# Kernel optimization log

Measured on AMD Instinct MI355X. Metric: run time of the kernel, lower is better.

Reference implementation:

```python
import jax, jax.numpy as jnp
import numpy as np

B, S, D, H = 2, 4096, 512, 8
HD = D // H
SCALE = float(np.sqrt(HD))


def setup_inputs() -> dict:
    key = jax.random.key(0)
    ks = jax.random.split(key, 11)
    std = 1.0 / np.sqrt(D)
    inp = {
        "query": jax.random.normal(ks[0], (B, S, D), jnp.float32),
        "key": jax.random.normal(ks[1], (B, S, D), jnp.float32),
        "value": jax.random.normal(ks[2], (B, S, D), jnp.float32),
        "Wq": jax.random.normal(ks[3], (D, D), jnp.float32) * std,
        "bq": jnp.zeros((D,), jnp.float32),
        "Wk": jax.random.normal(ks[4], (D, D), jnp.float32) * std,
        "bk": jnp.zeros((D,), jnp.float32),
        "Wv": jax.random.normal(ks[5], (D, D), jnp.float32) * std,
        "bv": jnp.zeros((D,), jnp.float32),
        "Wo": jax.random.normal(ks[6], (D, D), jnp.float32) * std,
        "bo": jnp.zeros((D,), jnp.float32),
    }
    return inp


def reference(query, key, value, Wq, bq, Wk, bk, Wv, bv, Wo, bo):
    # Linear projections, split into heads: [B, H, S, HD]
    def proj(x, W, b):
        y = jnp.einsum('bsd,df->bsf', x, W) + b
        return y.reshape(B, -1, H, HD).transpose(0, 2, 1, 3)

    Q = proj(query, Wq, bq)
    K = proj(key, Wk, bk)
    V = proj(value, Wv, bv)

    # Full [B, H, S, S] score matrix (faithful to the naive original)
    scores = jnp.einsum('bhqd,bhkd->bhqk', Q, K) / SCALE
    attn = jax.nn.softmax(scores, axis=-1)  # dropout = identity in eval
    attended = jnp.einsum('bhqk,bhkd->bhqd', attn, V)
    attended = attended.transpose(0, 2, 1, 3).reshape(B, -1, D)
    return jnp.einsum('bsd,df->bsf', attended, Wo) + bo
```

## Files before the change

### kernel.cpp

```cpp
#include <hip/hip_runtime.h>

typedef short short8 __attribute__((ext_vector_type(8)));
typedef short short4v __attribute__((ext_vector_type(4)));
typedef float f32x4 __attribute__((ext_vector_type(4)));
typedef float f32x16 __attribute__((ext_vector_type(16)));
typedef unsigned uint2v __attribute__((ext_vector_type(2)));

typedef __attribute__((address_space(1))) void gvoid;
typedef __attribute__((address_space(3))) void lvoid;

#define DEV static __device__ __forceinline__

constexpr int Dm = 512;
constexpr int Sm = 4096;
constexpr int Hh = 8;
constexpr long NTe = (long)2 * Sm * Dm;

#define QSCALE 0.18033688011112042f

DEV short f2bf(float f) {
  union { float f; unsigned u; } v; v.f = f;
  unsigned r = v.u + 0x7FFFu + ((v.u >> 16) & 1u);
  return (short)(r >> 16);
}

DEV float bf2f(short s) {
  unsigned u = ((unsigned)(unsigned short)s) << 16;
  union { unsigned u; float f; } v; v.u = u;
  return v.f;
}

DEV float exp2_fast(float x) {
#if __has_builtin(__builtin_amdgcn_exp2f)
  return __builtin_amdgcn_exp2f(x);
#else
  return exp2f(x);
#endif
}

DEV float max3f(float a, float b, float c) { return fmaxf(fmaxf(a, b), c); }

DEV unsigned cvt_pk_bf16(float lo, float hi) {
  unsigned r;
  asm("v_cvt_pk_bf16_f32 %0, %1, %2" : "=v"(r) : "v"(lo), "v"(hi));
  return r;
}

DEV int fr(int r) { return (r & 7) ^ (((r >> 3) & 1) << 2); }

DEV uint2v pl32swap(unsigned a, unsigned b) {
  return __builtin_amdgcn_permlane32_swap(a, b, false, false);
}
DEV float swap_max(float x) { return fmaxf(x, __shfl_xor(x, 32, 64)); }
DEV float swap_add(float x) { return x + __shfl_xor(x, 32, 64); }

DEV void async16(const void* g, void* l) {
  __builtin_amdgcn_global_load_lds((gvoid*)g, (lvoid*)l, 16, 0, 0);
}

__global__ __launch_bounds__(256) void cast_qkv(
    const float* __restrict__ q, const float* __restrict__ k,
    const float* __restrict__ v, short* __restrict__ xq,
    short* __restrict__ xk, short* __restrict__ xv) {
  int t = blockIdx.y;
  const float* src = (t == 0) ? q : (t == 1) ? k : v;
  short* dst = (t == 0) ? xq : (t == 1) ? xk : xv;
  long i = (long)(blockIdx.x * 256 + threadIdx.x) * 4;
  float4 f = *(const float4*)(src + i);
  short4v o;
  o[0] = f2bf(f.x); o[1] = f2bf(f.y); o[2] = f2bf(f.z); o[3] = f2bf(f.w);
  *(short4v*)(dst + i) = o;
}

__global__ __launch_bounds__(256) void wtrans(
    const float* __restrict__ wq, const float* __restrict__ wk,
    const float* __restrict__ wv, const float* __restrict__ wo,
    short* __restrict__ wt) {
  __shared__ short T[64 * 72];
  const int tid = threadIdx.x;
  const int n0 = blockIdx.x * 64, k0 = blockIdx.y * 64, w = blockIdx.z;
  const float* W = (w == 0) ? wq : (w == 1) ? wk : (w == 2) ? wv : wo;
  for (int t = 0; t < 4; ++t) {
    int flat = t * 256 + tid;
    int r = flat >> 4, c4 = flat & 15;
    float4 f = *(const float4*)(W + (k0 + r) * 512 + n0 + c4 * 4);
    T[(c4 * 4 + 0) * 72 + r] = f2bf(f.x);
    T[(c4 * 4 + 1) * 72 + r] = f2bf(f.y);
    T[(c4 * 4 + 2) * 72 + r] = f2bf(f.z);
    T[(c4 * 4 + 3) * 72 + r] = f2bf(f.w);
  }
  __syncthreads();
  for (int t = 0; t < 2; ++t) {
    int flat = t * 256 + tid;
    int r = flat >> 3, c = flat & 7;
    short8 v = *(const short8*)(T + r * 72 + c * 8);
    *(short8*)(wt + ((long)w << 18) + (n0 + r) * 512 + k0 + c * 8) = v;
  }
}

__global__ __launch_bounds__(256) void vtrans(
    const short* __restrict__ V, short* __restrict__ VT) {
  __shared__ short T[64 * 72];
  const int tid = threadIdx.x;
  const int s0 = blockIdx.x * 64, d0 = blockIdx.y * 64, b = blockIdx.z;
  for (int t = 0; t < 2; ++t) {
    int flat = t * 256 + tid;
    int sl = flat >> 3, c = flat & 7;
    short8 v = *(const short8*)(V + ((long)b * Sm + s0 + sl) * Dm + d0 + c * 8);
    for (int j = 0; j < 8; ++j) T[(c * 8 + j) * 72 + sl] = v[j];
  }
  __syncthreads();
  for (int t = 0; t < 2; ++t) {
    int flat = t * 256 + tid;
    int dl = flat >> 3, c = flat & 7;
    short8 v = *(const short8*)(T + dl * 72 + c * 8);
    *(short8*)(VT + ((long)b * Dm + d0 + dl) * Sm + s0 + c * 8) = v;
  }
}

template <bool OUT_BF16>
DEV void gemm_body(const short* __restrict__ A, const short* __restrict__ Bt,
                   const float* __restrict__ bias, float scale,
                   void* __restrict__ Yv, short* As, short* Bs) {
  constexpr int K = 512, N = 512, BK = 64;
  const int tid = threadIdx.x, lane = tid & 63, w = tid >> 6;
  const int lm = lane & 15, lg = lane >> 4;
  const int wr = w >> 1, wc = w & 1;
  const long bm = (long)blockIdx.y * 128;
  const long bn = (long)blockIdx.x * 128;
  f32x4 zero = {0.f, 0.f, 0.f, 0.f};
  f32x4 acc[4][4];
  for (int m = 0; m < 4; ++m)
    for (int n = 0; n < 4; ++n) acc[m][n] = zero;
  for (int k0 = 0; k0 < K; k0 += BK) {
    __syncthreads();
    for (int t = 0; t < 4; ++t) {
      int flat = t * 256 + tid;
      int row = flat >> 3, c = flat & 7;
      async16(A + (bm + row) * K + k0 + ((c ^ fr(row)) * 8), As + flat * 8);
    }
    for (int t = 0; t < 4; ++t) {
      int flat = t * 256 + tid;
      int row = flat >> 3, c = flat & 7;
      async16(Bt + (bn + row) * K + k0 + ((c ^ fr(row)) * 8), Bs + flat * 8);
    }
    __syncthreads();
    for (int kk = 0; kk < 2; ++kk) {
      short8 a[4], b[4];
      for (int m = 0; m < 4; ++m)
        a[m] = *(const short8*)(As + (wr * 64 + m * 16 + lm) * BK +
                                ((kk * 4 + lg) ^ fr(lm)) * 8);
      for (int n = 0; n < 4; ++n)
        b[n] = *(const short8*)(Bs + (wc * 64 + n * 16 + lm) * BK +
                                ((kk * 4 + lg) ^ fr(lm)) * 8);
      for (int m = 0; m < 4; ++m)
        for (int n = 0; n < 4; ++n)
          acc[m][n] = __builtin_amdgcn_mfma_f32_16x16x32_bf16(a[m], b[n], acc[m][n], 0, 0, 0);
    }
  }
  for (int m = 0; m < 4; ++m)
    for (int n = 0; n < 4; ++n) {
      long row0 = bm + wr * 64 + m * 16 + lg * 4;
      int col = (int)bn + wc * 64 + n * 16 + lm;
      float bb = bias[col];
      for (int j = 0; j < 4; ++j) {
        float val = (acc[m][n][j] + bb) * scale;
        if (OUT_BF16)
          ((short*)Yv)[(row0 + j) * N + col] = f2bf(val);
        else
          ((float*)Yv)[(row0 + j) * N + col] = val;
      }
    }
}

__global__ __launch_bounds__(256) void gemm_proj(
    const short* __restrict__ Xq, const short* __restrict__ Xk,
    const short* __restrict__ Xv, const short* __restrict__ Wt,
    const float* __restrict__ bq, const float* __restrict__ bk,
    const float* __restrict__ bv, short* __restrict__ Qb,
    short* __restrict__ Kb, short* __restrict__ Vb) {
  __shared__ short As[128 * 64];
  __shared__ short Bs[128 * 64];
  int z = blockIdx.z;
  const short* A = (z == 0) ? Xq : (z == 1) ? Xk : Xv;
  const short* Bt = Wt + (long)z * 512 * 512;
  const float* bias = (z == 0) ? bq : (z == 1) ? bk : bv;
  short* Y = (z == 0) ? Qb : (z == 1) ? Kb : Vb;
  float scale = (z == 0) ? QSCALE : 1.f;
  gemm_body<true>(A, Bt, bias, scale, Y, As, Bs);
}

__global__ __launch_bounds__(256) void gemm_out(
    const short* __restrict__ A, const short* __restrict__ Bt,
    const float* __restrict__ bias, float* __restrict__ Y) {
  __shared__ short As[128 * 64];
  __shared__ short Bs[128 * 64];
  gemm_body<false>(A, Bt, bias, 1.f, Y, As, Bs);
}

template <int NSPLIT>
__global__ __launch_bounds__(256) void attn(
    const short* __restrict__ Qb, const short* __restrict__ Kb,
    const short* __restrict__ VTb, short* __restrict__ Op0,
    short* __restrict__ OpRest, float2* __restrict__ Ml) {
  __shared__ short Ks[2][64 * 64];
  __shared__ short Vt[2][64 * 64];
  const int tid = threadIdx.x, lane = tid & 63, w = tid >> 6;
  const int q32 = lane & 31, l5 = lane >> 5;
  const int bh = blockIdx.y, b = bh >> 3, h = bh & 7;
  const int z = blockIdx.z;
  constexpr int KVLEN = Sm / NSPLIT;
  const int kvbase = z * KVLEN;
  const long baseQ = (long)b * Sm * Dm + h * 64;
  const long baseVT = ((long)b * Dm + h * 64) * Sm;
  const int q0w = blockIdx.x * 128 + w * 32;

  short8 qf[4];
#pragma unroll
  for (int ks = 0; ks < 4; ++ks)
    qf[ks] = *(const short8*)(Qb + baseQ + (long)(q0w + q32) * Dm + ks * 16 + l5 * 8);

  f32x16 o0, o1;
#pragma unroll
  for (int r = 0; r < 16; ++r) { o0[r] = 0.f; o1[r] = 0.f; }
  float mrun = -1e30f, lrun = 0.f;

  const int r0 = tid >> 3, c0 = tid & 7;
  const int r1 = 32 + (tid >> 3);
  const short* gk0 = Kb + baseQ + (long)(kvbase + r0) * Dm + (c0 ^ fr(r0)) * 8;
  const short* gk1 = Kb + baseQ + (long)(kvbase + r1) * Dm + (c0 ^ fr(r1)) * 8;
  const short* gv0 = VTb + baseVT + (long)r0 * Sm + kvbase + (c0 ^ fr(r0)) * 8;
  const short* gv1 = VTb + baseVT + (long)r1 * Sm + kvbase + (c0 ^ fr(r1)) * 8;
  const int l0 = tid * 8, l1 = (256 + tid) * 8;

  async16(gk0, &Ks[0][l0]); async16(gk1, &Ks[0][l1]);
  async16(gv0, &Vt[0][l0]); async16(gv1, &Vt[0][l1]);
  gk0 += 64 * Dm; gk1 += 64 * Dm; gv0 += 64; gv1 += 64;
  __syncthreads();

  const int cxor = fr(q32);

  constexpr int NTILES = KVLEN / 64;
  for (int it = 0; it < NTILES; ++it) {
    const int cur = it & 1;
    if (it + 1 < NTILES) {
      async16(gk0, &Ks[cur ^ 1][l0]); async16(gk1, &Ks[cur ^ 1][l1]);
      async16(gv0, &Vt[cur ^ 1][l0]); async16(gv1, &Vt[cur ^ 1][l1]);
      gk0 += 64 * Dm; gk1 += 64 * Dm; gv0 += 64; gv1 += 64;
    }

    f32x16 sc0, sc1;
#pragma unroll
    for (int r = 0; r < 16; ++r) { sc0[r] = 0.f; sc1[r] = 0.f; }
    __builtin_amdgcn_s_setprio(1);
#pragma unroll
    for (int ks = 0; ks < 4; ++ks) {
      int cx = (2 * ks + l5) ^ cxor;
      short8 kf0 = *(const short8*)(&Ks[cur][q32 * 64 + cx * 8]);
      short8 kf1 = *(const short8*)(&Ks[cur][(32 + q32) * 64 + cx * 8]);
      sc0 = __builtin_amdgcn_mfma_f32_32x32x16_bf16(kf0, qf[ks], sc0, 0, 0, 0);
      sc1 = __builtin_amdgcn_mfma_f32_32x32x16_bf16(kf1, qf[ks], sc1, 0, 0, 0);
    }
    __builtin_amdgcn_s_setprio(0);

    float t1 = max3f(sc0[0], sc0[1], sc0[2]);
    float t2 = max3f(sc0[3], sc0[4], sc0[5]);
    float t3 = max3f(sc0[6], sc0[7], sc0[8]);
    float t4 = max3f(sc0[9], sc0[10], sc0[11]);
    float t5 = max3f(sc0[12], sc0[13], sc0[14]);
    float ma = max3f(max3f(t1, t2, t3), max3f(t4, t5, sc0[15]), sc1[0]);
    t1 = max3f(sc1[1], sc1[2], sc1[3]);
    t2 = max3f(sc1[4], sc1[5], sc1[6]);
    t3 = max3f(sc1[7], sc1[8], sc1[9]);
    t4 = max3f(sc1[10], sc1[11], sc1[12]);
    t5 = max3f(sc1[13], sc1[14], sc1[15]);
    float tmax = fmaxf(ma, max3f(max3f(t1, t2, t3), t4, t5));
    tmax = swap_max(tmax);

    if (__any(tmax > mrun + 8.f)) {
      float mi = fmaxf(mrun, tmax);
      float cc = exp2_fast(mrun - mi);
      mrun = mi;
      lrun *= cc;
#pragma unroll
      for (int r = 0; r < 16; ++r) {
        float ccr = __shfl(cc, ((r & 3) + 8 * (r >> 2)) + 4 * l5, 32);
        o0[r] *= ccr;
        o1[r] *= ccr;
      }
    }

    float la[4] = {0.f, 0.f, 0.f, 0.f}, lb[4] = {0.f, 0.f, 0.f, 0.f};
#pragma unroll
    for (int r = 0; r < 16; ++r) {
      sc0[r] = exp2_fast(sc0[r] - mrun); la[r & 3] += sc0[r];
      sc1[r] = exp2_fast(sc1[r] - mrun); lb[r & 3] += sc1[r];
    }
    lrun += ((la[0] + la[1]) + (la[2] + la[3])) +
            ((lb[0] + lb[1]) + (lb[2] + lb[3]));

    __builtin_amdgcn_s_setprio(1);
#pragma unroll
    for (int kc = 0; kc < 4; ++kc) {
      const f32x16& sch = (kc < 2) ? sc0 : sc1;
      const int bb = 8 * (kc & 1);
      unsigned A = cvt_pk_bf16(sch[bb + 0], sch[bb + 1]);
      unsigned B = cvt_pk_bf16(sch[bb + 2], sch[bb + 3]);
      unsigned C = cvt_pk_bf16(sch[bb + 4], sch[bb + 5]);
      unsigned D = cvt_pk_bf16(sch[bb + 6], sch[bb + 7]);
      uint2v rac = pl32swap(A, C);
      uint2v rbd = pl32swap(B, D);
      union { unsigned u[4]; short8 s; } pu;
      pu.u[0] = rac[0]; pu.u[1] = rbd[0]; pu.u[2] = rac[1]; pu.u[3] = rbd[1];
      int cx = (2 * kc + l5) ^ cxor;
      short8 vf0 = *(const short8*)(&Vt[cur][q32 * 64 + cx * 8]);
      short8 vf1 = *(const short8*)(&Vt[cur][(32 + q32) * 64 + cx * 8]);
      o0 = __builtin_amdgcn_mfma_f32_32x32x16_bf16(pu.s, vf0, o0, 0, 0, 0);
      o1 = __builtin_amdgcn_mfma_f32_32x32x16_bf16(pu.s, vf1, o1, 0, 0, 0);
    }
    __builtin_amdgcn_s_setprio(0);
    __syncthreads();
  }

  lrun = swap_add(lrun);

  short* Op = (z == 0) ? Op0 : OpRest + (long)(z - 1) * NTe;
#pragma unroll
  for (int r = 0; r < 16; ++r) {
    int q = (r & 3) + 8 * (r >> 2) + 4 * l5;
    long rowoff = baseQ + (long)(q0w + q) * Dm;
    Op[rowoff + q32] = f2bf(o0[r]);
    Op[rowoff + 32 + q32] = f2bf(o1[r]);
  }
  if (l5 == 0) {
    float2 ml; ml.x = mrun; ml.y = lrun;
    Ml[(long)(z * 16 + bh) * Sm + q0w + q32] = ml;
  }
}

template <int NSPLIT>
__global__ __launch_bounds__(256) void mergeN(
    const short* __restrict__ Op0, const short* __restrict__ OpRest,
    const float2* __restrict__ Ml, short* __restrict__ Ob) {
  long idx = (long)blockIdx.x * 256 + threadIdx.x;
  long row = idx >> 6;
  int c8 = (int)(idx & 63);
  int col = c8 * 8;
  int h = col >> 6;
  int b = (int)(row >> 12);
  int s = (int)(row & 4095);
  int bh = b * 8 + h;
  float2 ml[NSPLIT];
  float M = -3e38f;
#pragma unroll
  for (int z = 0; z < NSPLIT; ++z) {
    ml[z] = Ml[(long)(z * 16 + bh) * Sm + s];
    M = fmaxf(M, ml[z].x);
  }
  float wz[NSPLIT], den = 0.f;
#pragma unroll
  for (int z = 0; z < NSPLIT; ++z) {
    wz[z] = exp2_fast(ml[z].x - M);
    den += ml[z].y * wz[z];
  }
  float inv = 1.0f / den;
  long off = row * 512 + col;
  float acc[8];
#pragma unroll
  for (int i = 0; i < 8; ++i) acc[i] = 0.f;
#pragma unroll
  for (int z = 0; z < NSPLIT; ++z) {
    const short* Op = (z == 0) ? Op0 : OpRest + (long)(z - 1) * NTe;
    short8 v = *(const short8*)(Op + off);
#pragma unroll
    for (int i = 0; i < 8; ++i) acc[i] += bf2f(v[i]) * wz[z];
  }
  short8 o;
#pragma unroll
  for (int i = 0; i < 8; ++i) o[i] = f2bf(acc[i] * inv);
  *(short8*)(Ob + off) = o;
}

extern "C" void kernel_launch(void* const* d_in, const int* in_sizes, int n_in,
                              void* d_out, int out_size, void* d_ws, size_t ws_size,
                              hipStream_t stream) {
  const float* query = (const float*)d_in[0];
  const float* key_  = (const float*)d_in[1];
  const float* value = (const float*)d_in[2];
  const float* Wq = (const float*)d_in[3]; const float* bq = (const float*)d_in[4];
  const float* Wk = (const float*)d_in[5]; const float* bk = (const float*)d_in[6];
  const float* Wv = (const float*)d_in[7]; const float* bv = (const float*)d_in[8];
  const float* Wo = (const float*)d_in[9]; const float* bo = (const float*)d_in[10];

  short* Xq = (short*)d_ws;
  short* Xk = Xq + NTe;
  short* Xv = Xk + NTe;
  short* Wt = Xv + NTe;
  short* Qb = Wt + 4 * 512 * 512;
  short* Kb = Qb + NTe;
  short* Vb = Kb + NTe;
  short* VT = Xv;
  short* Op0 = Xq;
  short* OpRest = Vb + NTe;
  short* Ob = Vb;

  const size_t base_bytes = (size_t)(6 * NTe + 4 * 512 * 512) * 2;
  const size_t need4 = base_bytes + 3 * (size_t)NTe * 2 + (size_t)4 * 16 * Sm * 8;
  const int nsplit = (ws_size >= need4) ? 4 : 2;
  float2* Ml = (float2*)(OpRest + (size_t)(nsplit - 1) * NTe);

  cast_qkv<<<dim3(4096, 3), 256, 0, stream>>>(query, key_, value, Xq, Xk, Xv);
  wtrans<<<dim3(8, 8, 4), 256, 0, stream>>>(Wq, Wk, Wv, Wo, Wt);

  gemm_proj<<<dim3(4, 64, 3), 256, 0, stream>>>(Xq, Xk, Xv, Wt, bq, bk, bv,
                                                Qb, Kb, Vb);

  vtrans<<<dim3(Sm / 64, Dm / 64, 2), 256, 0, stream>>>(Vb, VT);

  if (nsplit == 4) {
    attn<4><<<dim3(Sm / 128, 2 * Hh, 4), 256, 0, stream>>>(Qb, Kb, VT, Op0,
                                                           OpRest, Ml);
    mergeN<4><<<dim3((2 * Sm * 512 / 8) / 256), 256, 0, stream>>>(Op0, OpRest,
                                                                  Ml, Ob);
  } else {
    attn<2><<<dim3(Sm / 128, 2 * Hh, 2), 256, 0, stream>>>(Qb, Kb, VT, Op0,
                                                           OpRest, Ml);
    mergeN<2><<<dim3((2 * Sm * 512 / 8) / 256), 256, 0, stream>>>(Op0, OpRest,
                                                                  Ml, Ob);
  }

  gemm_out<<<dim3(4, 64), 256, 0, stream>>>(Ob, Wt + 3L * 512 * 512, bo,
                                            (float*)d_out);
}
```

Baseline: 179.2 us.

## Fuse split-KV merge into output projection GEMM A-tile load

Removes the separate mergeN kernel and its bf16 round-trip by merging the split-KV partial outputs with log-sum-exp weights directly while loading the A tile of the output projection GEMM. Also defers the cross-half max shuffle in attention to inside the rescale branch. The fused GEMM now loads A synchronously with per-row merge math that is recomputed once per N-tile (4x redundant reads of partials and Ml), trading a launch and an intermediate write/read for extra loads and less overlap.

After: 190.7 us. 1.06x slower.

```diff
diff --git a/kernel.cpp b/kernel.cpp
--- a/kernel.cpp
+++ b/kernel.cpp
@@ -190,12 +190,89 @@
   gemm_body<true>(A, Bt, bias, scale, Y, As, Bs);
 }
 
-__global__ __launch_bounds__(256) void gemm_out(
-    const short* __restrict__ A, const short* __restrict__ Bt,
+template <int NSPLIT>
+__global__ __launch_bounds__(256) void gemm_out_fused(
+    const short* __restrict__ Op0, const short* __restrict__ OpRest,
+    const float2* __restrict__ Ml, const short* __restrict__ Bt,
     const float* __restrict__ bias, float* __restrict__ Y) {
+  constexpr int K = 512, N = 512, BK = 64;
   __shared__ short As[128 * 64];
   __shared__ short Bs[128 * 64];
-  gemm_body<false>(A, Bt, bias, 1.f, Y, As, Bs);
+  const int tid = threadIdx.x, lane = tid & 63, w = tid >> 6;
+  const int lm = lane & 15, lg = lane >> 4;
+  const int wr = w >> 1, wc = w & 1;
+  const long bm = (long)blockIdx.y * 128;
+  const long bn = (long)blockIdx.x * 128;
+  f32x4 zero = {0.f, 0.f, 0.f, 0.f};
+  f32x4 acc[4][4];
+  for (int m = 0; m < 4; ++m)
+    for (int n = 0; n < 4; ++n) acc[m][n] = zero;
+  for (int k0 = 0; k0 < K; k0 += BK) {
+    __syncthreads();
+    const int hh = k0 >> 6;
+    for (int t = 0; t < 4; ++t) {
+      int flat = t * 256 + tid;
+      int row = flat >> 3, c = flat & 7;
+      long grow = bm + row;
+      int s = (int)(grow & (Sm - 1));
+      int bh = (int)(grow >> 12) * 8 + hh;
+      float2 ml[NSPLIT];
+      float M = -3e38f;
+#pragma unroll
+      for (int z = 0; z < NSPLIT; ++z) {
+        ml[z] = Ml[(long)(z * 16 + bh) * Sm + s];
+        M = fmaxf(M, ml[z].x);
+      }
+      float wz[NSPLIT], den = 0.f;
+#pragma unroll
+      for (int z = 0; z < NSPLIT; ++z) {
+        wz[z] = exp2_fast(ml[z].x - M);
+        den += ml[z].y * wz[z];
+      }
+      float inv = 1.0f / den;
+      long aoff = grow * 512 + k0 + ((c ^ fr(row)) * 8);
+      float accm[8];
+#pragma unroll
+      for (int i = 0; i < 8; ++i) accm[i] = 0.f;
+#pragma unroll
+      for (int z = 0; z < NSPLIT; ++z) {
+        const short* Op = (z == 0) ? Op0 : OpRest + (long)(z - 1) * NTe;
+        short8 v = *(const short8*)(Op + aoff);
+#pragma unroll
+        for (int i = 0; i < 8; ++i) accm[i] += bf2f(v[i]) * wz[z];
+      }
+      short8 o;
+#pragma unroll
+      for (int i = 0; i < 8; ++i) o[i] = f2bf(accm[i] * inv);
+      *(short8*)(As + flat * 8) = o;
+    }
+    for (int t = 0; t < 4; ++t) {
+      int flat = t * 256 + tid;
+      int row = flat >> 3, c = flat & 7;
+      async16(Bt + (bn + row) * K + k0 + ((c ^ fr(row)) * 8), Bs + flat * 8);
+    }
+    __syncthreads();
+    for (int kk = 0; kk < 2; ++kk) {
+      short8 a[4], b[4];
+      for (int m = 0; m < 4; ++m)
+        a[m] = *(const short8*)(As + (wr * 64 + m * 16 + lm) * BK +
+                                ((kk * 4 + lg) ^ fr(lm)) * 8);
+      for (int n = 0; n < 4; ++n)
+        b[n] = *(const short8*)(Bs + (wc * 64 + n * 16 + lm) * BK +
+                                ((kk * 4 + lg) ^ fr(lm)) * 8);
+      for (int m = 0; m < 4; ++m)
+        for (int n = 0; n < 4; ++n)
+          acc[m][n] = __builtin_amdgcn_mfma_f32_16x16x32_bf16(a[m], b[n], acc[m][n], 0, 0, 0);
+    }
+  }
+  for (int m = 0; m < 4; ++m)
+    for (int n = 0; n < 4; ++n) {
+      long row0 = bm + wr * 64 + m * 16 + lg * 4;
+      int col = (int)bn + wc * 64 + n * 16 + lm;
+      float bb = bias[col];
+      for (int j = 0; j < 4; ++j)
+        Y[(row0 + j) * N + col] = acc[m][n][j] + bb;
+    }
 }
 
 template <int NSPLIT>
@@ -274,10 +351,10 @@
     t3 = max3f(sc1[7], sc1[8], sc1[9]);
     t4 = max3f(sc1[10], sc1[11], sc1[12]);
     t5 = max3f(sc1[13], sc1[14], sc1[15]);
-    float tmax = fmaxf(ma, max3f(max3f(t1, t2, t3), t4, t5));
-    tmax = swap_max(tmax);
-
-    if (__any(tmax > mrun + 8.f)) {
+    float tmax_lane = fmaxf(ma, max3f(max3f(t1, t2, t3), t4, t5));
+
+    if (__any(tmax_lane > mrun + 8.f)) {
+      float tmax = swap_max(tmax_lane);
       float mi = fmaxf(mrun, tmax);
       float cc = exp2_fast(mrun - mi);
       mrun = mi;
@@ -338,49 +415,6 @@
   }
 }
 
-template <int NSPLIT>
-__global__ __launch_bounds__(256) void mergeN(
-    const short* __restrict__ Op0, const short* __restrict__ OpRest,
-    const float2* __restrict__ Ml, short* __restrict__ Ob) {
-  long idx = (long)blockIdx.x * 256 + threadIdx.x;
-  long row = idx >> 6;
-  int c8 = (int)(idx & 63);
-  int col = c8 * 8;
-  int h = col >> 6;
-  int b = (int)(row >> 12);
-  int s = (int)(row & 4095);
-  int bh = b * 8 + h;
-  float2 ml[NSPLIT];
-  float M = -3e38f;
-#pragma unroll
-  for (int z = 0; z < NSPLIT; ++z) {
-    ml[z] = Ml[(long)(z * 16 + bh) * Sm + s];
-    M = fmaxf(M, ml[z].x);
-  }
-  float wz[NSPLIT], den = 0.f;
-#pragma unroll
-  for (int z = 0; z < NSPLIT; ++z) {
-    wz[z] = exp2_fast(ml[z].x - M);
-    den += ml[z].y * wz[z];
-  }
-  float inv = 1.0f / den;
-  long off = row * 512 + col;
-  float acc[8];
-#pragma unroll
-  for (int i = 0; i < 8; ++i) acc[i] = 0.f;
-#pragma unroll
-  for (int z = 0; z < NSPLIT; ++z) {
-    const short* Op = (z == 0) ? Op0 : OpRest + (long)(z - 1) * NTe;
-    short8 v = *(const short8*)(Op + off);
-#pragma unroll
-    for (int i = 0; i < 8; ++i) acc[i] += bf2f(v[i]) * wz[z];
-  }
-  short8 o;
-#pragma unroll
-  for (int i = 0; i < 8; ++i) o[i] = f2bf(acc[i] * inv);
-  *(short8*)(Ob + off) = o;
-}
-
 extern "C" void kernel_launch(void* const* d_in, const int* in_sizes, int n_in,
                               void* d_out, int out_size, void* d_ws, size_t ws_size,
                               hipStream_t stream) {
@@ -402,7 +436,6 @@
   short* VT = Xv;
   short* Op0 = Xq;
   short* OpRest = Vb + NTe;
-  short* Ob = Vb;
 
   const size_t base_bytes = (size_t)(6 * NTe + 4 * 512 * 512) * 2;
   const size_t need4 = base_bytes + 3 * (size_t)NTe * 2 + (size_t)4 * 16 * Sm * 8;
@@ -420,15 +453,12 @@
   if (nsplit == 4) {
     attn<4><<<dim3(Sm / 128, 2 * Hh, 4), 256, 0, stream>>>(Qb, Kb, VT, Op0,
                                                            OpRest, Ml);
-    mergeN<4><<<dim3((2 * Sm * 512 / 8) / 256), 256, 0, stream>>>(Op0, OpRest,
-                                                                  Ml, Ob);
+    gemm_out_fused<4><<<dim3(4, 64), 256, 0, stream>>>(
+        Op0, OpRest, Ml, Wt + 3L * 512 * 512, bo, (float*)d_out);
   } else {
     attn<2><<<dim3(Sm / 128, 2 * Hh, 2), 256, 0, stream>>>(Qb, Kb, VT, Op0,
                                                            OpRest, Ml);
-    mergeN<2><<<dim3((2 * Sm * 512 / 8) / 256), 256, 0, stream>>>(Op0, OpRest,
-                                                                  Ml, Ob);
-  }
-
-  gemm_out<<<dim3(4, 64), 256, 0, stream>>>(Ob, Wt + 3L * 512 * 512, bo,
-                                            (float*)d_out);
-}
+    gemm_out_fused<2><<<dim3(4, 64), 256, 0, stream>>>(
+        Op0, OpRest, Ml, Wt + 3L * 512 * 512, bo, (float*)d_out);
+  }
+}
```

## Prefetch two KV tiles per barrier with quad-buffered shared memory

Applied to the files above, without the earlier changes.

The attention loop now processes two 64-row KV tiles between barriers. It keeps four LDS buffers for K and V and prefetches the next pair of tiles while computing the current pair, which halves the number of __syncthreads calls and lengthens the prefetch distance. The cross-lane swap_max is also moved inside the rare rescale branch, so it runs only when a rescale happens. This doubles LDS use per block to 64 KB, which may reduce occupancy. The loop also assumes NTILES is even.

After: 173.8 us. 1.03x faster.

```diff
diff --git a/kernel.cpp b/kernel.cpp
--- a/kernel.cpp
+++ b/kernel.cpp
@@ -203,8 +203,8 @@
     const short* __restrict__ Qb, const short* __restrict__ Kb,
     const short* __restrict__ VTb, short* __restrict__ Op0,
     short* __restrict__ OpRest, float2* __restrict__ Ml) {
-  __shared__ short Ks[2][64 * 64];
-  __shared__ short Vt[2][64 * 64];
+  __shared__ short Ks[4][64 * 64];
+  __shared__ short Vt[4][64 * 64];
   const int tid = threadIdx.x, lane = tid & 63, w = tid >> 6;
   const int q32 = lane & 31, l5 = lane >> 5;
   const int bh = blockIdx.y, b = bh >> 3, h = bh & 7;
@@ -233,22 +233,19 @@
   const short* gv1 = VTb + baseVT + (long)r1 * Sm + kvbase + (c0 ^ fr(r1)) * 8;
   const int l0 = tid * 8, l1 = (256 + tid) * 8;
 
-  async16(gk0, &Ks[0][l0]); async16(gk1, &Ks[0][l1]);
-  async16(gv0, &Vt[0][l0]); async16(gv1, &Vt[0][l1]);
-  gk0 += 64 * Dm; gk1 += 64 * Dm; gv0 += 64; gv1 += 64;
+  auto stage = [&](int buf) {
+    async16(gk0, &Ks[buf][l0]); async16(gk1, &Ks[buf][l1]);
+    async16(gv0, &Vt[buf][l0]); async16(gv1, &Vt[buf][l1]);
+    gk0 += 64 * Dm; gk1 += 64 * Dm; gv0 += 64; gv1 += 64;
+  };
+
+  stage(0);
+  stage(1);
   __syncthreads();
 
   const int cxor = fr(q32);
 
-  constexpr int NTILES = KVLEN / 64;
-  for (int it = 0; it < NTILES; ++it) {
-    const int cur = it & 1;
-    if (it + 1 < NTILES) {
-      async16(gk0, &Ks[cur ^ 1][l0]); async16(gk1, &Ks[cur ^ 1][l1]);
-      async16(gv0, &Vt[cur ^ 1][l0]); async16(gv1, &Vt[cur ^ 1][l1]);
-      gk0 += 64 * Dm; gk1 += 64 * Dm; gv0 += 64; gv1 += 64;
-    }
-
+  auto tile_body = [&](int buf) {
     f32x16 sc0, sc1;
 #pragma unroll
     for (int r = 0; r < 16; ++r) { sc0[r] = 0.f; sc1[r] = 0.f; }
@@ -256,8 +253,8 @@
 #pragma unroll
     for (int ks = 0; ks < 4; ++ks) {
       int cx = (2 * ks + l5) ^ cxor;
-      short8 kf0 = *(const short8*)(&Ks[cur][q32 * 64 + cx * 8]);
-      short8 kf1 = *(const short8*)(&Ks[cur][(32 + q32) * 64 + cx * 8]);
+      short8 kf0 = *(const short8*)(&Ks[buf][q32 * 64 + cx * 8]);
+      short8 kf1 = *(const short8*)(&Ks[buf][(32 + q32) * 64 + cx * 8]);
       sc0 = __builtin_amdgcn_mfma_f32_32x32x16_bf16(kf0, qf[ks], sc0, 0, 0, 0);
       sc1 = __builtin_amdgcn_mfma_f32_32x32x16_bf16(kf1, qf[ks], sc1, 0, 0, 0);
     }
@@ -274,10 +271,10 @@
     t3 = max3f(sc1[7], sc1[8], sc1[9]);
     t4 = max3f(sc1[10], sc1[11], sc1[12]);
     t5 = max3f(sc1[13], sc1[14], sc1[15]);
-    float tmax = fmaxf(ma, max3f(max3f(t1, t2, t3), t4, t5));
-    tmax = swap_max(tmax);
-
-    if (__any(tmax > mrun + 8.f)) {
+    float tmax_lane = fmaxf(ma, max3f(max3f(t1, t2, t3), t4, t5));
+
+    if (__any(tmax_lane > mrun + 8.f)) {
+      float tmax = swap_max(tmax_lane);
       float mi = fmaxf(mrun, tmax);
       float cc = exp2_fast(mrun - mi);
       mrun = mi;
@@ -313,12 +310,23 @@
       union { unsigned u[4]; short8 s; } pu;
       pu.u[0] = rac[0]; pu.u[1] = rbd[0]; pu.u[2] = rac[1]; pu.u[3] = rbd[1];
       int cx = (2 * kc + l5) ^ cxor;
-      short8 vf0 = *(const short8*)(&Vt[cur][q32 * 64 + cx * 8]);
-      short8 vf1 = *(const short8*)(&Vt[cur][(32 + q32) * 64 + cx * 8]);
+      short8 vf0 = *(const short8*)(&Vt[buf][q32 * 64 + cx * 8]);
+      short8 vf1 = *(const short8*)(&Vt[buf][(32 + q32) * 64 + cx * 8]);
       o0 = __builtin_amdgcn_mfma_f32_32x32x16_bf16(pu.s, vf0, o0, 0, 0, 0);
       o1 = __builtin_amdgcn_mfma_f32_32x32x16_bf16(pu.s, vf1, o1, 0, 0, 0);
     }
     __builtin_amdgcn_s_setprio(0);
+  };
+
+  constexpr int NTILES = KVLEN / 64;
+  for (int it = 0; it < NTILES; it += 2) {
+    const int p2 = (it >> 1) & 1;
+    if (it + 2 < NTILES) {
+      stage(2 * (1 - p2));
+      stage(2 * (1 - p2) + 1);
+    }
+    tile_body(2 * p2);
+    tile_body(2 * p2 + 1);
     __syncthreads();
   }
 
```
